# Kernel optimization log

Hardware: AMD Instinct MI355X
Metric: run time of the kernel (lower is better)

## Reference

```python
import jax, jax.numpy as jnp
import numpy as np

N_NODES = 100_000
N_EDGES = 1_600_000
N_GRAPHS = 256          # num_segments for batch scatter (static)
T_CAPS = 16             # num_target_cap
IN_CH = 64
OUT_CH = 64
NUM_ROUTES = 3
BN_EPS = 1e-5


def squash(s, axis=-1):
    # v = (|s|^2 / (1+|s|^2)) * s / |s|
    sq = jnp.sum(s * s, axis=axis, keepdims=True)
    return (sq / (1.0 + sq)) * s / jnp.sqrt(sq + 1e-16)


def setup_inputs() -> dict:
    key = jax.random.key(0)
    k_x, k_ei, k_ew, k_b, k_w, k_bias = jax.random.split(key, 6)
    x = jax.random.normal(k_x, (N_NODES, IN_CH), dtype=jnp.float32)
    edge_index = jax.random.randint(k_ei, (2, N_EDGES), 0, N_NODES, dtype=jnp.int32)
    edge_weight = jax.random.uniform(k_ew, (N_EDGES,), dtype=jnp.float32)
    batch = jnp.sort(jax.random.randint(k_b, (N_NODES,), 0, N_GRAPHS, dtype=jnp.int32))
    # per-capsule GCNConv weights, stacked: (T, in, out), bias (T, out)
    W = jax.random.normal(k_w, (T_CAPS, IN_CH, OUT_CH), dtype=jnp.float32) * 0.05
    bias = jax.random.normal(k_bias, (T_CAPS, OUT_CH), dtype=jnp.float32) * 0.05
    bn_gamma = jnp.ones((IN_CH,), dtype=jnp.float32)
    bn_beta = jnp.zeros((IN_CH,), dtype=jnp.float32)
    return {"x": x, "edge_index": edge_index, "edge_weight": edge_weight,
            "batch": batch, "bn_gamma": bn_gamma, "bn_beta": bn_beta,
            "W": W, "bias": bias}


def reference(x, edge_index, edge_weight, batch, bn_gamma, bn_beta, W, bias):
    N = x.shape[0]
    T = W.shape[0]
    # --- BatchNorm1d (training-mode batch statistics, biased variance) ---
    mu = jnp.mean(x, axis=0)
    var = jnp.var(x, axis=0)
    xn = (x - mu) * jax.lax.rsqrt(var + BN_EPS) * bn_gamma + bn_beta

    # --- GCNConv (shared graph): A_hat x, then per-capsule linear ---
    row, col = edge_index[0], edge_index[1]
    ar = jnp.arange(N, dtype=edge_index.dtype)
    row_f = jnp.concatenate([row, ar])              # add self-loops, weight 1
    col_f = jnp.concatenate([col, ar])
    w_f = jnp.concatenate([edge_weight, jnp.ones((N,), x.dtype)])
    deg = jax.ops.segment_sum(w_f, col_f, num_segments=N)
    dinv = jnp.where(deg > 0, jax.lax.rsqrt(deg), 0.0)
    norm = dinv[row_f] * w_f * dinv[col_f]          # (E+N,)
    h = jax.ops.segment_sum(norm[:, None] * xn[row_f], col_f, num_segments=N)  # (N, in)
    # linearity: propagate(A, x W_t) == (propagate(A, x)) W_t
    u_hat = jnp.einsum('ni,tio->nto', h, W) + bias[None]  # (N, T, D)

    # --- dynamic routing ---
    node_deg = jax.ops.segment_sum(edge_weight, row, num_segments=N)  # (N,)
    b_log = jnp.broadcast_to(node_deg[:, None, None], (N, T, 1))
    u_det = jax.lax.stop_gradient(u_hat)
    for _ in range(NUM_ROUTES - 1):
        c = jax.nn.softmax(b_log, axis=1)                         # (N, T, 1)
        s = jax.ops.segment_sum(c * u_det, batch, num_segments=N_GRAPHS)  # (G, T, D)
        v = squash(s, axis=-1)
        vg = v[batch]                                             # (N, T, D)
        b_log = b_log + jnp.sum(u_det * vg, axis=-1, keepdims=True)
    c = jax.nn.softmax(b_log, axis=1)
    s = jax.ops.segment_sum(c * u_hat, batch, num_segments=N_GRAPHS)  # (G, T, D)

    # --- add per-graph mean of (normalized) node features ---
    cnt = jax.ops.segment_sum(jnp.ones((N,), x.dtype), batch, num_segments=N_GRAPHS)
    x_mean = jax.ops.segment_sum(xn, batch, num_segments=N_GRAPHS) / jnp.maximum(cnt, 1.0)[:, None]
    s = s + x_mean[:, None, :]                                    # needs in==out
    v = squash(s, axis=-1)

    # --- final_layer=True: v.norm(p=-1, dim=-1) = (sum |v|^-1)^-1 ---
    out = 1.0 / jnp.sum(1.0 / jnp.abs(v), axis=-1)                # (G, T)
    return out
```

## Files before the change

### kernel.cpp

```cpp
#include <hip/hip_runtime.h>
#include <hip/hip_fp16.h>
#include <math.h>

#define N_NODES 100000
#define N_EDGES 1600000
#define N_GRAPHS 256
#define T_CAPS 16
#define D_CH 64
#define BN_EPS 1e-5f
#define NSPLIT 8
#define CHUNK 32
#define FIX_SCALE 33554432.0f
#define NB 782
#define EPB 4096
#define NBLK 391
#define NBN 512

__device__ __forceinline__ float waveReduceSum(float v) {
    for (int m = 32; m >= 1; m >>= 1) v += __shfl_xor(v, m, 64);
    return v;
}

__global__ void setup_kernel(float* bn_sums, float* hsum, float* xsum,
                             const float* __restrict__ W, float* __restrict__ WT,
                             const int* __restrict__ batch, int* __restrict__ gstart) {
    int idx = blockIdx.x * blockDim.x + threadIdx.x;
    if (idx < 128) bn_sums[idx] = 0.0f;
    if (idx < N_GRAPHS * D_CH) { hsum[idx] = 0.0f; xsum[idx] = 0.0f; }
    if (idx < T_CAPS * 64 * 64) {
        int t = idx >> 12, rem = idx & 4095, o = rem >> 6, i = rem & 63;
        WT[idx] = W[t * 4096 + i * 64 + o];
    }
    if (idx <= N_GRAPHS) {
        int lo = 0, hi = N_NODES;
        while (lo < hi) { int mid = (lo + hi) >> 1; if (batch[mid] < idx) lo = mid + 1; else hi = mid; }
        gstart[idx] = lo;
    }
}

__global__ void passA_bn_kernel(const int* __restrict__ col, int* __restrict__ gh,
                                const float* __restrict__ x, float* __restrict__ sums,
                                __half2* __restrict__ x16) {
    int blk = blockIdx.x;
    int tid = threadIdx.x;
    if (blk < NBLK) {
        __shared__ unsigned hist[NB];
        for (int j = tid; j < NB; j += 256) hist[j] = 0u;
        __syncthreads();
        #pragma unroll
        for (int i = 0; i < EPB / 256; i++) {
            int e = blk * EPB + i * 256 + tid;
            if (e < N_EDGES) atomicAdd(&hist[col[e] >> 7], 1u);
        }
        __syncthreads();
        for (int j = tid; j < NB; j += 256) gh[blk * NB + j] = (int)hist[j];
    } else {
        int bb = blk - NBLK;
        int pr = tid & 31;
        int rg = tid >> 5;
        int c0 = pr * 2;
        float s0 = 0, q0 = 0, s1 = 0, q1 = 0;
        for (int r = bb * 8 + rg; r < N_NODES; r += NBN * 8) {
            float2 v = *(const float2*)(x + (size_t)r * 64 + c0);
            s0 += v.x; q0 += v.x * v.x;
            s1 += v.y; q1 += v.y * v.y;
            x16[(size_t)r * 32 + pr] = __floats2half2_rn(v.x, v.y);
        }
        __shared__ float ls[2][8][64];
        ls[0][rg][c0] = s0; ls[0][rg][c0 + 1] = s1;
        ls[1][rg][c0] = q0; ls[1][rg][c0 + 1] = q1;
        __syncthreads();
        if (tid < 64) {
            float a = 0.0f, bsm = 0.0f;
            for (int i = 0; i < 8; i++) { a += ls[0][i][tid]; bsm += ls[1][i][tid]; }
            atomicAdd(&sums[tid], a);
            atomicAdd(&sums[64 + tid], bsm);
        }
    }
}

__global__ void passB1_kernel(int* __restrict__ gh, int* __restrict__ Tarr) {
    int b = blockIdx.x;
    int tid = threadIdx.x;
    __shared__ int lds[256];
    int i0 = tid * 2, i1 = tid * 2 + 1;
    int v0 = (i0 < NBLK) ? gh[(size_t)i0 * NB + b] : 0;
    int v1 = (i1 < NBLK) ? gh[(size_t)i1 * NB + b] : 0;
    int pair = v0 + v1;
    lds[tid] = pair;
    __syncthreads();
    for (int d = 1; d < 256; d <<= 1) {
        int v = (tid >= d) ? lds[tid - d] : 0;
        __syncthreads();
        lds[tid] += v;
        __syncthreads();
    }
    int excl = lds[tid] - pair;
    if (i0 < NBLK) gh[(size_t)i0 * NB + b] = excl;
    if (i1 < NBLK) gh[(size_t)i1 * NB + b] = excl + v0;
    if (tid == 255) Tarr[b] = lds[255];
}

__global__ void passB2_kernel(const int* __restrict__ Tarr, int* __restrict__ Sarr,
                              int* __restrict__ off) {
    __shared__ int lds[256];
    int tid = threadIdx.x;
    int base = tid * 4;
    int t0 = (base + 0 < NB) ? Tarr[base + 0] : 0;
    int t1 = (base + 1 < NB) ? Tarr[base + 1] : 0;
    int t2 = (base + 2 < NB) ? Tarr[base + 2] : 0;
    int t3 = (base + 3 < NB) ? Tarr[base + 3] : 0;
    int tsum = t0 + t1 + t2 + t3;
    lds[tid] = tsum;
    __syncthreads();
    for (int d = 1; d < 256; d <<= 1) {
        int v = (tid >= d) ? lds[tid - d] : 0;
        __syncthreads();
        lds[tid] += v;
        __syncthreads();
    }
    int excl = lds[tid] - tsum;
    if (base + 0 < NB) Sarr[base + 0] = excl;
    if (base + 1 < NB) Sarr[base + 1] = excl + t0;
    if (base + 2 < NB) Sarr[base + 2] = excl + t0 + t1;
    if (base + 3 < NB) Sarr[base + 3] = excl + t0 + t1 + t2;
    if (tid == 0) { Sarr[NB] = N_EDGES; off[N_NODES] = N_EDGES; }
}

__global__ void passC_kernel(const int* __restrict__ row, const int* __restrict__ col,
                             const float* __restrict__ ew, const int* __restrict__ gh,
                             const int* __restrict__ Sarr, int2* __restrict__ brec) {
    int blk = blockIdx.x;
    int tid = threadIdx.x;
    __shared__ int cur[NB];
    for (int j = tid; j < NB; j += 256) cur[j] = Sarr[j] + gh[(size_t)blk * NB + j];
    __syncthreads();
    #pragma unroll
    for (int i = 0; i < EPB / 256; i++) {
        int e = blk * EPB + i * 256 + tid;
        if (e < N_EDGES) {
            int c = col[e], r = row[e];
            float w = ew[e];
            int b = c >> 7;
            int pos = atomicAdd(&cur[b], 1);
            brec[pos] = make_int2(((c & 127) << 17) | r, __float_as_int(w));
        }
    }
}

__global__ void passD_kernel(const int2* __restrict__ brec, const int* __restrict__ Sarr,
                             float* __restrict__ dinv, int* __restrict__ off,
                             int2* __restrict__ rec) {
    int b = blockIdx.x;
    int tid = threadIdx.x;
    int s0 = Sarr[b], s1 = Sarr[b + 1];
    __shared__ unsigned cnt[128];
    __shared__ unsigned degfx[128];
    __shared__ int scan_tmp[128];
    __shared__ int cOff[128];
    __shared__ int cursor[128];
    if (tid < 128) { cnt[tid] = 0u; degfx[tid] = 0u; }
    __syncthreads();
    for (int e = s0 + tid; e < s1; e += 256) {
        int2 rc = brec[e];
        int cl = (rc.x >> 17) & 127;
        atomicAdd(&cnt[cl], 1u);
        unsigned fx = __float2uint_rn(__int_as_float(rc.y) * FIX_SCALE);
        atomicAdd(&degfx[cl], fx);
    }
    __syncthreads();
    if (tid < 128) scan_tmp[tid] = (int)cnt[tid];
    __syncthreads();
    for (int d = 1; d < 128; d <<= 1) {
        int v = 0;
        if (tid < 128 && tid >= d) v = scan_tmp[tid - d];
        __syncthreads();
        if (tid < 128) scan_tmp[tid] += v;
        __syncthreads();
    }
    if (tid < 128) {
        int excl = scan_tmp[tid] - (int)cnt[tid];
        cOff[tid] = excl;
        cursor[tid] = excl;
        int cg = b * 128 + tid;
        if (cg < N_NODES) {
            float d = 1.0f + (float)degfx[tid] * (1.0f / FIX_SCALE);
            dinv[cg] = 1.0f / sqrtf(d);
            off[cg] = s0 + excl;
        }
    }
    __syncthreads();
    for (int e = s0 + tid; e < s1; e += 256) {
        int2 rc = brec[e];
        int cl = (rc.x >> 17) & 127;
        int pos = atomicAdd((unsigned*)&cursor[cl], 1u);
        rec[s0 + (int)pos] = make_int2(rc.x & 0x1FFFF, rc.y);
    }
}

__global__ void h_gather_kernel(const int2* __restrict__ rec, const int* __restrict__ off,
                                const float* __restrict__ dinv, const __half* __restrict__ x16,
                                const float* __restrict__ ab, float* __restrict__ h) {
    int n = blockIdx.x * 4 + (threadIdx.x >> 6);
    int ch = threadIdx.x & 63;
    int e0 = off[n], e1 = off[n + 1];
    float dv = dinv[n];
    float cself = dv * dv;
    float acc0 = cself * __half2float(x16[(size_t)n * 64 + ch]);
    float acc1 = 0.0f, acc2 = 0.0f, acc3 = 0.0f;
    float csr = cself;
    int e = e0;
    for (; e + 4 <= e1; e += 4) {
        int2 r0 = rec[e], r1 = rec[e + 1], r2 = rec[e + 2], r3 = rec[e + 3];
        float c0 = dinv[r0.x] * __int_as_float(r0.y) * dv;
        float c1 = dinv[r1.x] * __int_as_float(r1.y) * dv;
        float c2 = dinv[r2.x] * __int_as_float(r2.y) * dv;
        float c3 = dinv[r3.x] * __int_as_float(r3.y) * dv;
        float x0 = __half2float(x16[(size_t)r0.x * 64 + ch]);
        float x1 = __half2float(x16[(size_t)r1.x * 64 + ch]);
        float x2 = __half2float(x16[(size_t)r2.x * 64 + ch]);
        float x3 = __half2float(x16[(size_t)r3.x * 64 + ch]);
        acc0 += c0 * x0; acc1 += c1 * x1; acc2 += c2 * x2; acc3 += c3 * x3;
        csr += c0 + c1 + c2 + c3;
    }
    for (; e < e1; ++e) {
        int2 rc = rec[e];
        float c = dinv[rc.x] * __int_as_float(rc.y) * dv;
        acc0 += c * __half2float(x16[(size_t)rc.x * 64 + ch]);
        csr += c;
    }
    float acc = (acc0 + acc1) + (acc2 + acc3);
    h[(size_t)n * 64 + ch] = ab[ch] * acc + ab[64 + ch] * csr;
}

__global__ void ab_kernel(const float* __restrict__ sums, const float* __restrict__ gamma,
                          const float* __restrict__ beta, float* __restrict__ ab) {
    int tid = threadIdx.x;
    if (tid < 64) {
        float mu = sums[tid] * (1.0f / N_NODES);
        float var = sums[64 + tid] * (1.0f / N_NODES) - mu * mu;
        float inv = 1.0f / sqrtf(var + BN_EPS);
        float a = inv * gamma[tid];
        ab[tid] = a;
        ab[64 + tid] = beta[tid] - mu * a;
    }
}

__global__ void gsum_kernel(const __half* __restrict__ x16, const float* __restrict__ h,
                            const int* __restrict__ gstart, float* __restrict__ xsum,
                            float* __restrict__ hsum) {
    int g = blockIdx.x / NSPLIT, sp = blockIdx.x % NSPLIT;
    int s0g = gstart[g], s1g = gstart[g + 1];
    int len = s1g - s0g;
    int q = (len + NSPLIT - 1) / NSPLIT;
    int a0 = s0g + sp * q, a1 = min(s1g, a0 + q);
    int ch = threadIdx.x & 63, rg = threadIdx.x >> 6;
    float ax = 0.0f, ah = 0.0f;
    for (int n = a0 + rg; n < a1; n += 4) {
        ax += __half2float(x16[(size_t)n * 64 + ch]);
        ah += h[(size_t)n * 64 + ch];
    }
    __shared__ float lx[4][64], lh[4][64];
    lx[rg][ch] = ax; lh[rg][ch] = ah;
    __syncthreads();
    if (threadIdx.x < 64) {
        int c = threadIdx.x;
        float sx = lx[0][c] + lx[1][c] + lx[2][c] + lx[3][c];
        float sh = lh[0][c] + lh[1][c] + lh[2][c] + lh[3][c];
        atomicAdd(&xsum[g * 64 + c], sx);
        atomicAdd(&hsum[g * 64 + c], sh);
    }
}

__global__ void ka_fused_kernel(const float* __restrict__ h, const int* __restrict__ gstart,
                                const float* __restrict__ wva, const float* __restrict__ bva,
                                const float* __restrict__ wvb, const float* __restrict__ bvb,
                                float* __restrict__ hc_part, float* __restrict__ csum_part,
                                int mode) {
    int g = blockIdx.x / NSPLIT, sp = blockIdx.x % NSPLIT;
    int s0g = gstart[g], s1g = gstart[g + 1];
    int len = s1g - s0g;
    int q = (len + NSPLIT - 1) / NSPLIT;
    int s0 = s0g + sp * q, s1 = min(s1g, s0 + q);
    int tid = threadIdx.x;
    int d = tid & 63, tg = tid >> 6;
    int t = tid & 15, kh = tid >> 4;

    __shared__ float hlds[CHUNK][65];
    __shared__ float wa[16][65];
    __shared__ float wb[16][65];
    __shared__ float clds[CHUNK][17];
    __shared__ float bvl[2][16];

    for (int i = tid; i < 16 * 64; i += 256) {
        int tt = i >> 6, dd = i & 63;
        wa[tt][dd] = wva[(g * 16 + tt) * 64 + dd];
        if (mode) wb[tt][dd] = wvb[(g * 16 + tt) * 64 + dd];
    }
    if (tid < 16) { bvl[0][tid] = bva[g * 16 + tid]; bvl[1][tid] = mode ? bvb[g * 16 + tid] : 0.0f; }
    for (int i = tid; i < CHUNK * 65; i += 256) ((float*)hlds)[i] = 0.0f;
    __syncthreads();

    float acc0 = 0, acc1 = 0, acc2 = 0, acc3 = 0;
    float cs0 = 0, cs1 = 0, cs2 = 0, cs3 = 0;

    for (int n0 = s0; n0 < s1; n0 += CHUNK) {
        int nn = min(CHUNK, s1 - n0);
        #pragma unroll
        for (int j = 0; j < 8; j++) {
            int k = tg * 8 + j;
            if (k < nn) hlds[k][d] = h[(size_t)(n0 + k) * 64 + d];
        }
        __syncthreads();
        int k0 = kh, k1 = kh + 16;
        float u0, u1;
        if (mode) {
            float a0 = bvl[0][t], a1 = bvl[0][t], b0 = bvl[1][t], b1 = bvl[1][t];
            for (int dd = 0; dd < 64; dd++) {
                float wav = wa[t][dd], wbv = wb[t][dd];
                float h0 = hlds[k0][dd], h1 = hlds[k1][dd];
                a0 += h0 * wav; a1 += h1 * wav;
                b0 += h0 * wbv; b1 += h1 * wbv;
            }
            u0 = a0 + b0; u1 = a1 + b1;
        } else {
            float a0 = bvl[0][t], a1 = bvl[0][t];
            for (int dd = 0; dd < 64; dd++) {
                float wav = wa[t][dd];
                a0 += hlds[k0][dd] * wav; a1 += hlds[k1][dd] * wav;
            }
            u0 = a0; u1 = a1;
        }
        float m0 = u0, m1 = u1;
        #pragma unroll
        for (int msk = 1; msk < 16; msk <<= 1) {
            m0 = fmaxf(m0, __shfl_xor(m0, msk, 64));
            m1 = fmaxf(m1, __shfl_xor(m1, msk, 64));
        }
        float e0 = expf(u0 - m0), e1 = expf(u1 - m1);
        float z0 = e0, z1 = e1;
        #pragma unroll
        for (int msk = 1; msk < 16; msk <<= 1) {
            z0 += __shfl_xor(z0, msk, 64);
            z1 += __shfl_xor(z1, msk, 64);
        }
        if (k0 < nn) clds[k0][t] = e0 / z0;
        if (k1 < nn) clds[k1][t] = e1 / z1;
        __syncthreads();
        for (int k = 0; k < nn; k++) {
            float hv = hlds[k][d];
            float c0 = clds[k][tg * 4 + 0], c1 = clds[k][tg * 4 + 1];
            float c2 = clds[k][tg * 4 + 2], c3 = clds[k][tg * 4 + 3];
            acc0 += c0 * hv; acc1 += c1 * hv; acc2 += c2 * hv; acc3 += c3 * hv;
            if (d == 0) { cs0 += c0; cs1 += c1; cs2 += c2; cs3 += c3; }
        }
        __syncthreads();
    }
    size_t base = ((size_t)(sp * N_GRAPHS + g) * 16 + tg * 4) * 64 + d;
    hc_part[base] = acc0; hc_part[base + 64] = acc1;
    hc_part[base + 128] = acc2; hc_part[base + 192] = acc3;
    if (d == 0) {
        int cb = (sp * N_GRAPHS + g) * 16 + tg * 4;
        csum_part[cb + 0] = cs0; csum_part[cb + 1] = cs1;
        csum_part[cb + 2] = cs2; csum_part[cb + 3] = cs3;
    }
}

__global__ void kb_kernel(const float* __restrict__ hsum, const float* __restrict__ hc_part,
                          const float* __restrict__ csum_part, const float* __restrict__ W,
                          const float* __restrict__ WT, const float* __restrict__ bias,
                          const float* __restrict__ xsum, const float* __restrict__ ab,
                          const int* __restrict__ gstart, float* __restrict__ wv,
                          float* __restrict__ bv, float* __restrict__ out, int mode) {
    int wid = blockIdx.x * 4 + (threadIdx.x >> 6);
    int lane = threadIdx.x & 63;
    int g = wid >> 4, t = wid & 15;
    const float* Wt = W + t * 4096;
    float cnt = (float)(gstart[g + 1] - gstart[g]);
    float s;
    if (mode == 0) {
        const float* hr = hsum + g * 64;
        float acc = cnt * bias[t * 64 + lane];
        for (int i = 0; i < 64; i++) acc += hr[i] * Wt[i * 64 + lane];
        s = acc * (1.0f / 16.0f);
    } else {
        float csum = 0.0f;
        #pragma unroll
        for (int sp = 0; sp < NSPLIT; sp++) csum += csum_part[(sp * N_GRAPHS + g) * 16 + t];
        float acc = csum * bias[t * 64 + lane];
        for (int i = 0; i < 64; i++) {
            float hci = 0.0f;
            #pragma unroll
            for (int sp = 0; sp < NSPLIT; sp++)
                hci += hc_part[((size_t)(sp * N_GRAPHS + g) * 16 + t) * 64 + i];
            acc += hci * Wt[i * 64 + lane];
        }
        s = acc;
        if (mode == 2) {
            float xm = ab[lane] * xsum[g * 64 + lane] / fmaxf(cnt, 1.0f) + ab[64 + lane];
            s += xm;
        }
    }
    float sq = waveReduceSum(s * s);
    float scale = (sq / (1.0f + sq)) / sqrtf(sq + 1e-16f);
    float v = scale * s;
    if (mode == 2) {
        float tot = waveReduceSum(1.0f / fabsf(v));
        if (lane == 0) out[wid] = 1.0f / tot;
    } else {
        __shared__ float vlds[4][64];
        int w = threadIdx.x >> 6;
        vlds[w][lane] = v;
        __syncthreads();
        const float* WTt = WT + t * 4096;
        float acc = 0.0f;
        for (int o = 0; o < 64; o++) acc += WTt[o * 64 + lane] * vlds[w][o];
        wv[(size_t)wid * 64 + lane] = acc;
        float b = waveReduceSum(bias[t * 64 + lane] * v);
        if (lane == 0) bv[wid] = b;
    }
}

extern "C" void kernel_launch(void* const* d_in, const int* in_sizes, int n_in,
                              void* d_out, int out_size, void* d_ws, size_t ws_size,
                              hipStream_t stream) {
    const float* x     = (const float*)d_in[0];
    const int*   ei    = (const int*)d_in[1];
    const float* ew    = (const float*)d_in[2];
    const int*   batch = (const int*)d_in[3];
    const float* gamma = (const float*)d_in[4];
    const float* beta  = (const float*)d_in[5];
    const float* W     = (const float*)d_in[6];
    const float* bias  = (const float*)d_in[7];
    float* out = (float*)d_out;

    const int* row = ei;
    const int* col = ei + N_EDGES;

    char* basep = (char*)d_ws;
    int2* rec  = (int2*)basep;                     basep += sizeof(int2) * N_EDGES;
    int2* brec = (int2*)basep;                     basep += sizeof(int2) * N_EDGES;
    __half2* x16 = (__half2*)basep;                basep += 2ULL * N_NODES * D_CH;
    float* p = (float*)basep;
    float* h        = p; p += (size_t)N_NODES * D_CH;
    float* hc_part  = p; p += (size_t)NSPLIT * N_GRAPHS * T_CAPS * D_CH;
    float* csum_part= p; p += NSPLIT * N_GRAPHS * T_CAPS;
    float* wva      = p; p += N_GRAPHS * T_CAPS * D_CH;
    float* bva      = p; p += N_GRAPHS * T_CAPS;
    float* wvb      = p; p += N_GRAPHS * T_CAPS * D_CH;
    float* bvb      = p; p += N_GRAPHS * T_CAPS;
    float* WT       = p; p += T_CAPS * 64 * 64;
    float* dinv     = p; p += N_NODES;
    float* bn_sums  = p; p += 128;
    float* ab       = p; p += 128;
    float* hsum     = p; p += N_GRAPHS * D_CH;
    float* xsum     = p; p += N_GRAPHS * D_CH;
    int*   ip       = (int*)p;
    int*   off      = ip; ip += N_NODES + 1;
    int*   gh       = ip; ip += (size_t)NBLK * NB;
    int*   Tarr     = ip; ip += NB;
    int*   Sarr     = ip; ip += NB + 1;
    int*   gstart   = ip; ip += N_GRAPHS + 1;

    setup_kernel<<<(T_CAPS * 64 * 64 + 255) / 256, 256, 0, stream>>>(bn_sums, hsum, xsum,
                                                                      W, WT, batch, gstart);
    passA_bn_kernel<<<NBLK + NBN, 256, 0, stream>>>(col, gh, x, bn_sums, x16);
    ab_kernel<<<1, 64, 0, stream>>>(bn_sums, gamma, beta, ab);
    passB1_kernel<<<NB, 256, 0, stream>>>(gh, Tarr);
    passB2_kernel<<<1, 256, 0, stream>>>(Tarr, Sarr, off);
    passC_kernel<<<NBLK, 256, 0, stream>>>(row, col, ew, gh, Sarr, brec);
    passD_kernel<<<NB, 256, 0, stream>>>(brec, Sarr, dinv, off, rec);
    h_gather_kernel<<<N_NODES / 4, 256, 0, stream>>>(rec, off, dinv, (const __half*)x16, ab, h);
    gsum_kernel<<<N_GRAPHS * NSPLIT, 256, 0, stream>>>((const __half*)x16, h, gstart, xsum, hsum);

    kb_kernel<<<N_GRAPHS * T_CAPS / 4, 256, 0, stream>>>(hsum, hc_part, csum_part, W, WT, bias,
                                                          xsum, ab, gstart, wva, bva, out, 0);
    ka_fused_kernel<<<N_GRAPHS * NSPLIT, 256, 0, stream>>>(h, gstart, wva, bva, wvb, bvb,
                                                            hc_part, csum_part, 0);
    kb_kernel<<<N_GRAPHS * T_CAPS / 4, 256, 0, stream>>>(hsum, hc_part, csum_part, W, WT, bias,
                                                          xsum, ab, gstart, wvb, bvb, out, 1);
    ka_fused_kernel<<<N_GRAPHS * NSPLIT, 256, 0, stream>>>(h, gstart, wva, bva, wvb, bvb,
                                                            hc_part, csum_part, 1);
    kb_kernel<<<N_GRAPHS * T_CAPS / 4, 256, 0, stream>>>(hsum, hc_part, csum_part, W, WT, bias,
                                                          xsum, ab, gstart, wva, bva, out, 2);
}
```

Before: 279.0 us.

## Store propagated features in fp16, fold BN-affine kernel into scan, unroll gather by 8

The aggregated node features h are now written and read as half precision, which halves their memory traffic in the gather write, the graph-sum pass and both routing passes. The standalone kernel that computes the batchnorm scale and shift is merged into the single-block prefix-scan kernel, removing one launch. The edge gather loop gains an 8-wide unrolled stage so more independent loads are in flight. The fp16 storage of h adds rounding error to the routing and output values.

```diff
diff --git a/kernel.cpp b/kernel.cpp
--- a/kernel.cpp
+++ b/kernel.cpp
@@ -102,9 +102,19 @@
 }
 
 __global__ void passB2_kernel(const int* __restrict__ Tarr, int* __restrict__ Sarr,
-                              int* __restrict__ off) {
+                              int* __restrict__ off, const float* __restrict__ sums,
+                              const float* __restrict__ gamma, const float* __restrict__ beta,
+                              float* __restrict__ ab) {
     __shared__ int lds[256];
     int tid = threadIdx.x;
+    if (tid < 64) {
+        float mu = sums[tid] * (1.0f / N_NODES);
+        float var = sums[64 + tid] * (1.0f / N_NODES) - mu * mu;
+        float inv = 1.0f / sqrtf(var + BN_EPS);
+        float a = inv * gamma[tid];
+        ab[tid] = a;
+        ab[64 + tid] = beta[tid] - mu * a;
+    }
     int base = tid * 4;
     int t0 = (base + 0 < NB) ? Tarr[base + 0] : 0;
     int t1 = (base + 1 < NB) ? Tarr[base + 1] : 0;
@@ -157,7 +167,6 @@
     __shared__ unsigned cnt[128];
     __shared__ unsigned degfx[128];
     __shared__ int scan_tmp[128];
-    __shared__ int cOff[128];
     __shared__ int cursor[128];
     if (tid < 128) { cnt[tid] = 0u; degfx[tid] = 0u; }
     __syncthreads();
@@ -180,7 +189,6 @@
     }
     if (tid < 128) {
         int excl = scan_tmp[tid] - (int)cnt[tid];
-        cOff[tid] = excl;
         cursor[tid] = excl;
         int cg = b * 128 + tid;
         if (cg < N_NODES) {
@@ -200,7 +208,7 @@
 
 __global__ void h_gather_kernel(const int2* __restrict__ rec, const int* __restrict__ off,
                                 const float* __restrict__ dinv, const __half* __restrict__ x16,
-                                const float* __restrict__ ab, float* __restrict__ h) {
+                                const float* __restrict__ ab, __half* __restrict__ h16) {
     int n = blockIdx.x * 4 + (threadIdx.x >> 6);
     int ch = threadIdx.x & 63;
     int e0 = off[n], e1 = off[n + 1];
@@ -210,6 +218,22 @@
     float acc1 = 0.0f, acc2 = 0.0f, acc3 = 0.0f;
     float csr = cself;
     int e = e0;
+    for (; e + 8 <= e1; e += 8) {
+        int2 r[8];
+        #pragma unroll
+        for (int i = 0; i < 8; i++) r[i] = rec[e + i];
+        float cf[8], xv[8];
+        #pragma unroll
+        for (int i = 0; i < 8; i++) {
+            cf[i] = dinv[r[i].x] * __int_as_float(r[i].y) * dv;
+            xv[i] = __half2float(x16[(size_t)r[i].x * 64 + ch]);
+        }
+        acc0 += cf[0] * xv[0]; acc1 += cf[1] * xv[1];
+        acc2 += cf[2] * xv[2]; acc3 += cf[3] * xv[3];
+        acc0 += cf[4] * xv[4]; acc1 += cf[5] * xv[5];
+        acc2 += cf[6] * xv[6]; acc3 += cf[7] * xv[7];
+        csr += ((cf[0] + cf[1]) + (cf[2] + cf[3])) + ((cf[4] + cf[5]) + (cf[6] + cf[7]));
+    }
     for (; e + 4 <= e1; e += 4) {
         int2 r0 = rec[e], r1 = rec[e + 1], r2 = rec[e + 2], r3 = rec[e + 3];
         float c0 = dinv[r0.x] * __int_as_float(r0.y) * dv;
@@ -230,23 +254,10 @@
         csr += c;
     }
     float acc = (acc0 + acc1) + (acc2 + acc3);
-    h[(size_t)n * 64 + ch] = ab[ch] * acc + ab[64 + ch] * csr;
-}
-
-__global__ void ab_kernel(const float* __restrict__ sums, const float* __restrict__ gamma,
-                          const float* __restrict__ beta, float* __restrict__ ab) {
-    int tid = threadIdx.x;
-    if (tid < 64) {
-        float mu = sums[tid] * (1.0f / N_NODES);
-        float var = sums[64 + tid] * (1.0f / N_NODES) - mu * mu;
-        float inv = 1.0f / sqrtf(var + BN_EPS);
-        float a = inv * gamma[tid];
-        ab[tid] = a;
-        ab[64 + tid] = beta[tid] - mu * a;
-    }
-}
-
-__global__ void gsum_kernel(const __half* __restrict__ x16, const float* __restrict__ h,
+    h16[(size_t)n * 64 + ch] = __float2half(ab[ch] * acc + ab[64 + ch] * csr);
+}
+
+__global__ void gsum_kernel(const __half* __restrict__ x16, const __half* __restrict__ h16,
                             const int* __restrict__ gstart, float* __restrict__ xsum,
                             float* __restrict__ hsum) {
     int g = blockIdx.x / NSPLIT, sp = blockIdx.x % NSPLIT;
@@ -258,7 +269,7 @@
     float ax = 0.0f, ah = 0.0f;
     for (int n = a0 + rg; n < a1; n += 4) {
         ax += __half2float(x16[(size_t)n * 64 + ch]);
-        ah += h[(size_t)n * 64 + ch];
+        ah += __half2float(h16[(size_t)n * 64 + ch]);
     }
     __shared__ float lx[4][64], lh[4][64];
     lx[rg][ch] = ax; lh[rg][ch] = ah;
@@ -272,7 +283,7 @@
     }
 }
 
-__global__ void ka_fused_kernel(const float* __restrict__ h, const int* __restrict__ gstart,
+__global__ void ka_fused_kernel(const __half* __restrict__ h16, const int* __restrict__ gstart,
                                 const float* __restrict__ wva, const float* __restrict__ bva,
                                 const float* __restrict__ wvb, const float* __restrict__ bvb,
                                 float* __restrict__ hc_part, float* __restrict__ csum_part,
@@ -309,7 +320,7 @@
         #pragma unroll
         for (int j = 0; j < 8; j++) {
             int k = tg * 8 + j;
-            if (k < nn) hlds[k][d] = h[(size_t)(n0 + k) * 64 + d];
+            if (k < nn) hlds[k][d] = __half2float(h16[(size_t)(n0 + k) * 64 + d]);
         }
         __syncthreads();
         int k0 = kh, k1 = kh + 16;
@@ -441,8 +452,8 @@
     int2* rec  = (int2*)basep;                     basep += sizeof(int2) * N_EDGES;
     int2* brec = (int2*)basep;                     basep += sizeof(int2) * N_EDGES;
     __half2* x16 = (__half2*)basep;                basep += 2ULL * N_NODES * D_CH;
+    __half* h16 = (__half*)basep;                  basep += 2ULL * N_NODES * D_CH;
     float* p = (float*)basep;
-    float* h        = p; p += (size_t)N_NODES * D_CH;
     float* hc_part  = p; p += (size_t)NSPLIT * N_GRAPHS * T_CAPS * D_CH;
     float* csum_part= p; p += NSPLIT * N_GRAPHS * T_CAPS;
     float* wva      = p; p += N_GRAPHS * T_CAPS * D_CH;
@@ -465,21 +476,20 @@
     setup_kernel<<<(T_CAPS * 64 * 64 + 255) / 256, 256, 0, stream>>>(bn_sums, hsum, xsum,
                                                                       W, WT, batch, gstart);
     passA_bn_kernel<<<NBLK + NBN, 256, 0, stream>>>(col, gh, x, bn_sums, x16);
-    ab_kernel<<<1, 64, 0, stream>>>(bn_sums, gamma, beta, ab);
     passB1_kernel<<<NB, 256, 0, stream>>>(gh, Tarr);
-    passB2_kernel<<<1, 256, 0, stream>>>(Tarr, Sarr, off);
+    passB2_kernel<<<1, 256, 0, stream>>>(Tarr, Sarr, off, bn_sums, gamma, beta, ab);
     passC_kernel<<<NBLK, 256, 0, stream>>>(row, col, ew, gh, Sarr, brec);
     passD_kernel<<<NB, 256, 0, stream>>>(brec, Sarr, dinv, off, rec);
-    h_gather_kernel<<<N_NODES / 4, 256, 0, stream>>>(rec, off, dinv, (const __half*)x16, ab, h);
-    gsum_kernel<<<N_GRAPHS * NSPLIT, 256, 0, stream>>>((const __half*)x16, h, gstart, xsum, hsum);
+    h_gather_kernel<<<N_NODES / 4, 256, 0, stream>>>(rec, off, dinv, (const __half*)x16, ab, h16);
+    gsum_kernel<<<N_GRAPHS * NSPLIT, 256, 0, stream>>>((const __half*)x16, h16, gstart, xsum, hsum);
 
     kb_kernel<<<N_GRAPHS * T_CAPS / 4, 256, 0, stream>>>(hsum, hc_part, csum_part, W, WT, bias,
                                                           xsum, ab, gstart, wva, bva, out, 0);
-    ka_fused_kernel<<<N_GRAPHS * NSPLIT, 256, 0, stream>>>(h, gstart, wva, bva, wvb, bvb,
+    ka_fused_kernel<<<N_GRAPHS * NSPLIT, 256, 0, stream>>>(h16, gstart, wva, bva, wvb, bvb,
                                                             hc_part, csum_part, 0);
     kb_kernel<<<N_GRAPHS * T_CAPS / 4, 256, 0, stream>>>(hsum, hc_part, csum_part, W, WT, bias,
                                                           xsum, ab, gstart, wvb, bvb, out, 1);
-    ka_fused_kernel<<<N_GRAPHS * NSPLIT, 256, 0, stream>>>(h, gstart, wva, bva, wvb, bvb,
+    ka_fused_kernel<<<N_GRAPHS * NSPLIT, 256, 0, stream>>>(h16, gstart, wva, bva, wvb, bvb,
                                                             hc_part, csum_part, 1);
     kb_kernel<<<N_GRAPHS * T_CAPS / 4, 256, 0, stream>>>(hsum, hc_part, csum_part, W, WT, bias,
                                                           xsum, ab, gstart, wva, bva, out, 2);
```

New measurement: 274.9 us. No clear change (-1.5%).
